# Kernel optimization log

Hardware: AMD Instinct MI355X
Metric: run time of the kernel (lower is better)

The kernel has to match this reference:

```python
import jax, jax.numpy as jnp
import numpy as np

B, S, D, H = 4, 2048, 1024, 16  # batch, seq, num_hiddens, heads
HD = D // H  # head dim = 64
MASK_VALUE = -1e6


def setup_inputs() -> dict:
    key = jax.random.key(0)
    ks = jax.random.split(key, 8)
    scale = 1.0 / np.sqrt(D)
    return {
        "queries": jax.random.normal(ks[0], (B, S, D), jnp.float32),
        "keys": jax.random.normal(ks[1], (B, S, D), jnp.float32),
        "values": jax.random.normal(ks[2], (B, S, D), jnp.float32),
        "valid_lens": jax.random.randint(ks[3], (B,), 1, S + 1, jnp.int32),
        # torch Linear weights: shape (out_features, in_features), y = x @ W.T
        "Wq": jax.random.uniform(ks[4], (D, D), jnp.float32, -scale, scale),
        "Wk": jax.random.uniform(ks[5], (D, D), jnp.float32, -scale, scale),
        "Wv": jax.random.uniform(ks[6], (D, D), jnp.float32, -scale, scale),
        "Wo": jax.random.uniform(ks[7], (D, D), jnp.float32, -scale, scale),
    }


def _split_heads(x):
    # (B, S, D) -> (B, H, S, HD)
    return x.reshape(B, S, H, HD).transpose(0, 2, 1, 3)


def reference(queries, keys, values, valid_lens, Wq, Wk, Wv, Wo):
    q = _split_heads(queries @ Wq.T)
    k = _split_heads(keys @ Wk.T)
    v = _split_heads(values @ Wv.T)
    scores = jnp.einsum("bhqd,bhkd->bhqk", q, k) / jnp.sqrt(jnp.float32(HD))
    # per-batch valid_len masks keys beyond valid_len (same for all heads/queries)
    key_pos = jnp.arange(S)
    mask = key_pos[None, None, None, :] < valid_lens[:, None, None, None]
    scores = jnp.where(mask, scores, MASK_VALUE)
    attn = jax.nn.softmax(scores, axis=-1)
    out = jnp.einsum("bhqk,bhkd->bhqd", attn, v)  # (B, H, S, HD)
    out = out.transpose(0, 2, 1, 3).reshape(B, S, D)
    return out @ Wo.T
```

## Files before the change

### kernel.cpp

```cpp
#include <hip/hip_runtime.h>

#define Bn 4
#define Sn 2048
#define Dn 1024
#define Hn 16
#define HDn 64

typedef unsigned short u16;
typedef unsigned int u32;
typedef __bf16 bf16x8 __attribute__((ext_vector_type(8)));
typedef float f32x4 __attribute__((ext_vector_type(4)));

__device__ __forceinline__ u32 pack_rne(float a, float b) {
    u32 ua = __float_as_uint(a); ua += 0x7fffu + ((ua >> 16) & 1u);
    u32 ub = __float_as_uint(b); ub += 0x7fffu + ((ub >> 16) & 1u);
    return __builtin_amdgcn_perm(ub, ua, 0x07060302u);
}
__device__ __forceinline__ u32 pack_trunc(float a, float b) {
    return __builtin_amdgcn_perm(__float_as_uint(b), __float_as_uint(a), 0x07060302u);
}

__device__ __forceinline__ void async_copy16(const u16* g, u16* l) {
    __builtin_amdgcn_global_load_lds(
        (__attribute__((address_space(1))) void*)(g),
        (__attribute__((address_space(3))) void*)(l), 16, 0, 0);
}

struct CvtArgs {
    const float* in[7];
    u16* out[7];
    int n4[7];
};
__global__ __launch_bounds__(256) void cvt_multi(CvtArgs a) {
    int s = blockIdx.y;
    const float4* in4 = (const float4*)a.in[s];
    uint2* out2 = (uint2*)a.out[s];
    int n4 = a.n4[s];
    int i = blockIdx.x * blockDim.x + threadIdx.x;
    int stride = gridDim.x * blockDim.x;
    for (; i < n4; i += stride) {
        float4 v = in4[i];
        out2[i] = make_uint2(pack_rne(v.x, v.y), pack_rne(v.z, v.w));
    }
}

struct GemmArgs {
    const u16* A[3];
    const u16* Bw[3];
    void* C[3];
    float scale[3];
    int mode[3];
};
template <int NZ>
__global__ __launch_bounds__(256, 3) void gemm_bf16(GemmArgs g) {
    __shared__ alignas(16) u16 As[128 * 64];
    __shared__ alignas(16) u16 Bs[128 * 64];
    u32 id = blockIdx.x;
    int xcd = id & 7;
    u32 s = id >> 3;
    int col0 = (int)(s & 7) * 128;
    u32 t2 = s >> 3;
    int z = (int)(t2 % NZ);
    int rg = (int)(t2 / NZ);
    int row0 = (rg * 8 + xcd) * 128;

    const u16* A = g.A[z];
    const u16* Bw = g.Bw[z];
    void* Cout = g.C[z];
    float scale = g.scale[z];
    int mode = g.mode[z];

    int t = threadIdx.x;
    int w = t >> 6, lane = t & 63;
    int lane15 = lane & 15, quad = lane >> 4;
    int wr = w >> 1, wc = w & 1;
    int sr = t >> 3, sg = t & 7;

    bool swapped = (mode != 3);
    const u16* PA = swapped ? Bs : As;
    const u16* PB = swapped ? As : Bs;
    int abase = swapped ? wc * 64 : wr * 64;
    int bbase = swapped ? wr * 64 : wc * 64;

    f32x4 acc[4][4];
#pragma unroll
    for (int mt = 0; mt < 4; ++mt)
#pragma unroll
        for (int nt = 0; nt < 4; ++nt)
            acc[mt][nt] = f32x4{0.f, 0.f, 0.f, 0.f};

    for (int k0 = 0; k0 < 1024; k0 += 64) {
        __syncthreads();
#pragma unroll
        for (int i = 0; i < 4; ++i) {
            int r = i * 32 + sr;
            int gc = ((sg ^ (r & 7)) << 3);
            const u16* ga = A + (size_t)(row0 + r) * 1024 + k0 + gc;
            const u16* gb = Bw + (size_t)(col0 + r) * 1024 + k0 + gc;
            async_copy16(ga, &As[i * 2048 + w * 512]);
            async_copy16(gb, &Bs[i * 2048 + w * 512]);
        }
        __syncthreads();

#pragma unroll
        for (int kc = 0; kc < 2; ++kc) {
            bf16x8 af[4], bf[4];
#pragma unroll
            for (int mt = 0; mt < 4; ++mt) {
                int r = abase + mt * 16 + lane15;
                af[mt] = *(const bf16x8*)&PA[r * 64 + (((kc * 4 + quad) ^ (r & 7)) << 3)];
            }
#pragma unroll
            for (int nt = 0; nt < 4; ++nt) {
                int r = bbase + nt * 16 + lane15;
                bf[nt] = *(const bf16x8*)&PB[r * 64 + (((kc * 4 + quad) ^ (r & 7)) << 3)];
            }
#pragma unroll
            for (int mt = 0; mt < 4; ++mt)
#pragma unroll
                for (int nt = 0; nt < 4; ++nt)
                    acc[mt][nt] = __builtin_amdgcn_mfma_f32_16x16x32_bf16(
                        af[mt], bf[nt], acc[mt][nt], 0, 0, 0);
        }
    }

#pragma unroll
    for (int mt = 0; mt < 4; ++mt)
#pragma unroll
        for (int nt = 0; nt < 4; ++nt) {
            if (mode == 1) {
                int f0 = col0 + wc * 64 + mt * 16 + quad * 4;
                int tok = row0 + wr * 64 + nt * 16 + lane15;
                int bb = tok >> 11, ss = tok & 2047;
                int hh = f0 >> 6, dd = f0 & 63;
                u32 w0 = pack_rne(acc[mt][nt][0] * scale, acc[mt][nt][1] * scale);
                u32 w1 = pack_rne(acc[mt][nt][2] * scale, acc[mt][nt][3] * scale);
                u16* p = (u16*)Cout + (((size_t)bb * Hn + hh) * Sn + ss) * HDn + dd;
                *(uint2*)p = make_uint2(w0, w1);
            } else if (mode == 2) {
                int f0 = col0 + wc * 64 + mt * 16 + quad * 4;
                int tok = row0 + wr * 64 + nt * 16 + lane15;
                float4 o = make_float4(acc[mt][nt][0] * scale, acc[mt][nt][1] * scale,
                                       acc[mt][nt][2] * scale, acc[mt][nt][3] * scale);
                *(float4*)((float*)Cout + (size_t)tok * 1024 + f0) = o;
            } else {
                int n = col0 + wc * 64 + nt * 16 + lane15;
                int m0 = row0 + wr * 64 + mt * 16 + quad * 4;
                int bb = m0 >> 11, ss = m0 & 2047;
                int hh = n >> 6, dd = n & 63;
                u32 w0 = pack_rne(acc[mt][nt][0] * scale, acc[mt][nt][1] * scale);
                u32 w1 = pack_rne(acc[mt][nt][2] * scale, acc[mt][nt][3] * scale);
                u16* p = (u16*)Cout + (((size_t)bb * Hn + hh) * HDn + dd) * Sn + ss;
                *(uint2*)p = make_uint2(w0, w1);
            }
        }
}

__global__ __launch_bounds__(256, 4) void attn_kernel(const u16* __restrict__ Qh,
                                                      const u16* __restrict__ Kh,
                                                      const u16* __restrict__ Vtg,
                                                      const int* __restrict__ valid_lens,
                                                      u16* __restrict__ O) {
    __shared__ alignas(16) u16 Ks[64 * 72];
    __shared__ alignas(16) u16 Vt[64 * 72];

    int t = threadIdx.x;
    int w = t >> 6, lane = t & 63;
    int lane15 = lane & 15, quad = lane >> 4;

    u32 raw = blockIdx.x;
    int qt = raw >> 6;
    int h = (raw >> 2) & 15;
    int b = (raw & 3) ^ ((raw >> 8) & 3);
    int bh = b * Hn + h;
    int q0 = qt * 128;
    int vl = valid_lens[b];
    int ntiles = (vl + 63) >> 6;

    const u16* Qb = Qh + (size_t)bh * (Sn * HDn);
    const u16* Kb = Kh + (size_t)bh * (Sn * HDn);
    const u16* Vb = Vtg + (size_t)bh * (HDn * Sn);

    int sr = t >> 3;
    int sc8 = (t & 7) * 8;
    int va = t & 7;
    int vcb = ((va & 4) << 3) | ((va & 1) << 4) | ((va & 2) << 1);

    bf16x8 qf[2][2];
#pragma unroll
    for (int nt = 0; nt < 2; ++nt)
#pragma unroll
        for (int kc = 0; kc < 2; ++kc)
            qf[nt][kc] = *(const bf16x8*)(Qb + (size_t)(q0 + w * 32 + nt * 16 + lane15) * HDn +
                                          kc * 32 + quad * 8);

    f32x4 oacc[4][2], lacc[2];
#pragma unroll
    for (int mt = 0; mt < 4; ++mt)
#pragma unroll
        for (int nt = 0; nt < 2; ++nt)
            oacc[mt][nt] = f32x4{0.f, 0.f, 0.f, 0.f};
    lacc[0] = f32x4{0.f, 0.f, 0.f, 0.f};
    lacc[1] = f32x4{0.f, 0.f, 0.f, 0.f};

    union { u32 u[4]; bf16x8 v; } ones;
    ones.u[0] = ones.u[1] = ones.u[2] = ones.u[3] = 0x3F803F80u;

    uint4 kpre[2], vpre[2];
#pragma unroll
    for (int p = 0; p < 2; ++p) {
        kpre[p] = *(const uint4*)(Kb + (size_t)(p * 32 + sr) * HDn + sc8);
        vpre[p] = *(const uint4*)(Vb + (size_t)(p * 32 + sr) * Sn + sc8);
    }

    for (int kt = 0; kt < ntiles; ++kt) {
        int kbase = kt * 64;
        __syncthreads();
#pragma unroll
        for (int p = 0; p < 2; ++p) {
            *(uint4*)&Ks[(p * 32 + sr) * 72 + sc8] = kpre[p];
            int drow = (p * 32 + sr) * 72;
            *(uint2*)&Vt[drow + vcb] = make_uint2(vpre[p].x, vpre[p].y);
            *(uint2*)&Vt[drow + vcb + 8] = make_uint2(vpre[p].z, vpre[p].w);
        }
        __syncthreads();

        int nkb = (kt + 1 < ntiles) ? kbase + 64 : kbase;
#pragma unroll
        for (int p = 0; p < 2; ++p) {
            kpre[p] = *(const uint4*)(Kb + (size_t)(nkb + p * 32 + sr) * HDn + sc8);
            vpre[p] = *(const uint4*)(Vb + (size_t)(p * 32 + sr) * Sn + nkb + sc8);
        }

        f32x4 sc[4][2];
#pragma unroll
        for (int mt = 0; mt < 4; ++mt) {
            bf16x8 kf0 = *(const bf16x8*)&Ks[(mt * 16 + lane15) * 72 + quad * 8];
            bf16x8 kf1 = *(const bf16x8*)&Ks[(mt * 16 + lane15) * 72 + 32 + quad * 8];
#pragma unroll
            for (int nt = 0; nt < 2; ++nt) {
                f32x4 s = f32x4{0.f, 0.f, 0.f, 0.f};
                s = __builtin_amdgcn_mfma_f32_16x16x32_bf16(kf0, qf[nt][0], s, 0, 0, 0);
                s = __builtin_amdgcn_mfma_f32_16x16x32_bf16(kf1, qf[nt][1], s, 0, 0, 0);
                sc[mt][nt] = s;
            }
        }

        if (kbase + 64 > vl) {
#pragma unroll
            for (int mt = 0; mt < 4; ++mt)
#pragma unroll
                for (int reg = 0; reg < 4; ++reg) {
                    int key = kbase + mt * 16 + quad * 4 + reg;
                    if (key >= vl) {
                        sc[mt][0][reg] = -1e30f;
                        sc[mt][1][reg] = -1e30f;
                    }
                }
        }

#pragma unroll
        for (int mt = 0; mt < 4; ++mt)
#pragma unroll
            for (int nt = 0; nt < 2; ++nt)
#pragma unroll
                for (int reg = 0; reg < 4; ++reg)
                    sc[mt][nt][reg] = __builtin_amdgcn_exp2f(sc[mt][nt][reg]);

        union { u32 u[4]; bf16x8 v; } pv[2][2];
#pragma unroll
        for (int nt = 0; nt < 2; ++nt) {
            pv[nt][0].u[0] = pack_trunc(sc[0][nt][0], sc[0][nt][1]);
            pv[nt][0].u[1] = pack_trunc(sc[0][nt][2], sc[0][nt][3]);
            pv[nt][0].u[2] = pack_trunc(sc[1][nt][0], sc[1][nt][1]);
            pv[nt][0].u[3] = pack_trunc(sc[1][nt][2], sc[1][nt][3]);
            pv[nt][1].u[0] = pack_trunc(sc[2][nt][0], sc[2][nt][1]);
            pv[nt][1].u[1] = pack_trunc(sc[2][nt][2], sc[2][nt][3]);
            pv[nt][1].u[2] = pack_trunc(sc[3][nt][0], sc[3][nt][1]);
            pv[nt][1].u[3] = pack_trunc(sc[3][nt][2], sc[3][nt][3]);
            lacc[nt] = __builtin_amdgcn_mfma_f32_16x16x32_bf16(
                ones.v, pv[nt][0].v, lacc[nt], 0, 0, 0);
            lacc[nt] = __builtin_amdgcn_mfma_f32_16x16x32_bf16(
                ones.v, pv[nt][1].v, lacc[nt], 0, 0, 0);
        }

#pragma unroll
        for (int mt = 0; mt < 4; ++mt) {
            bf16x8 vf0 = *(const bf16x8*)&Vt[(mt * 16 + lane15) * 72 + quad * 8];
            bf16x8 vf1 = *(const bf16x8*)&Vt[(mt * 16 + lane15) * 72 + 32 + quad * 8];
#pragma unroll
            for (int nt = 0; nt < 2; ++nt) {
                oacc[mt][nt] = __builtin_amdgcn_mfma_f32_16x16x32_bf16(
                    vf0, pv[nt][0].v, oacc[mt][nt], 0, 0, 0);
                oacc[mt][nt] = __builtin_amdgcn_mfma_f32_16x16x32_bf16(
                    vf1, pv[nt][1].v, oacc[mt][nt], 0, 0, 0);
            }
        }
    }

    float rl[2];
    rl[0] = __builtin_amdgcn_rcpf(lacc[0][0]);
    rl[1] = __builtin_amdgcn_rcpf(lacc[1][0]);
#pragma unroll
    for (int mt = 0; mt < 4; ++mt)
#pragma unroll
        for (int nt = 0; nt < 2; ++nt) {
            int q = q0 + w * 32 + nt * 16 + lane15;
            int d = h * HDn + mt * 16 + quad * 4;
            u32 w0 = pack_rne(oacc[mt][nt][0] * rl[nt], oacc[mt][nt][1] * rl[nt]);
            u32 w1 = pack_rne(oacc[mt][nt][2] * rl[nt], oacc[mt][nt][3] * rl[nt]);
            *(uint2*)&O[((size_t)b * Sn + q) * Dn + d] = make_uint2(w0, w1);
        }
}

extern "C" void kernel_launch(void* const* d_in, const int* in_sizes, int n_in,
                              void* d_out, int out_size, void* d_ws, size_t ws_size,
                              hipStream_t stream) {
    const float* q  = (const float*)d_in[0];
    const float* k  = (const float*)d_in[1];
    const float* v  = (const float*)d_in[2];
    const int*   vl = (const int*)d_in[3];
    const float* Wq = (const float*)d_in[4];
    const float* Wk = (const float*)d_in[5];
    const float* Wv = (const float*)d_in[6];
    const float* Wo = (const float*)d_in[7];

    u16* ws = (u16*)d_ws;
    const size_t NE = (size_t)Bn * Sn * Dn;
    const size_t NW = (size_t)Dn * Dn;
    const float qscale = 0.125f * 1.44269504f;

    if (ws_size >= (6 * NE + 4 * NW) * 2) {
        u16* Qh  = ws;
        u16* Kh  = Qh + NE;
        u16* Vh  = Kh + NE;
        u16* Xq  = Vh + NE;
        u16* Xk  = Xq + NE;
        u16* Xv  = Xk + NE;
        u16* Wqb = Xv + NE;
        u16* Wkb = Wqb + NW;
        u16* Wvb = Wkb + NW;
        u16* Wob = Wvb + NW;
        u16* Ob  = Xq;

        CvtArgs ca;
        ca.in[0] = q;  ca.out[0] = Xq;  ca.n4[0] = (int)(NE / 4);
        ca.in[1] = k;  ca.out[1] = Xk;  ca.n4[1] = (int)(NE / 4);
        ca.in[2] = v;  ca.out[2] = Xv;  ca.n4[2] = (int)(NE / 4);
        ca.in[3] = Wq; ca.out[3] = Wqb; ca.n4[3] = (int)(NW / 4);
        ca.in[4] = Wk; ca.out[4] = Wkb; ca.n4[4] = (int)(NW / 4);
        ca.in[5] = Wv; ca.out[5] = Wvb; ca.n4[5] = (int)(NW / 4);
        ca.in[6] = Wo; ca.out[6] = Wob; ca.n4[6] = (int)(NW / 4);
        cvt_multi<<<dim3(512, 7), 256, 0, stream>>>(ca);

        GemmArgs gp;
        gp.A[0] = Xq; gp.Bw[0] = Wqb; gp.C[0] = Qh; gp.scale[0] = qscale; gp.mode[0] = 1;
        gp.A[1] = Xk; gp.Bw[1] = Wkb; gp.C[1] = Kh; gp.scale[1] = 1.0f;   gp.mode[1] = 1;
        gp.A[2] = Xv; gp.Bw[2] = Wvb; gp.C[2] = Vh; gp.scale[2] = 1.0f;   gp.mode[2] = 3;
        gemm_bf16<3><<<dim3(1536), 256, 0, stream>>>(gp);

        attn_kernel<<<dim3(1024), 256, 0, stream>>>(Qh, Kh, Vh, vl, Ob);

        GemmArgs go;
        for (int i = 0; i < 3; ++i) {
            go.A[i] = Ob; go.Bw[i] = Wob; go.C[i] = d_out;
            go.scale[i] = 1.0f; go.mode[i] = 2;
        }
        gemm_bf16<1><<<dim3(512), 256, 0, stream>>>(go);
    } else {
        u16* Qh  = ws;
        u16* Kh  = Qh + NE;
        u16* Vh  = Kh + NE;
        u16* Xb  = Vh + NE;
        u16* Wqb = Xb + NE;
        u16* Wkb = Wqb + NW;
        u16* Wvb = Wkb + NW;
        u16* Wob = Wvb + NW;
        u16* Ob  = Wob + NW;

        CvtArgs cw;
        cw.in[0] = Wq; cw.out[0] = Wqb; cw.n4[0] = (int)(NW / 4);
        cw.in[1] = Wk; cw.out[1] = Wkb; cw.n4[1] = (int)(NW / 4);
        cw.in[2] = Wv; cw.out[2] = Wvb; cw.n4[2] = (int)(NW / 4);
        cw.in[3] = Wo; cw.out[3] = Wob; cw.n4[3] = (int)(NW / 4);
        for (int i = 4; i < 7; ++i) { cw.in[i] = Wq; cw.out[i] = Wqb; cw.n4[i] = 0; }
        cvt_multi<<<dim3(512, 4), 256, 0, stream>>>(cw);

        const float* xs[3] = {q, k, v};
        u16* outs[3] = {Qh, Kh, Vh};
        const u16* wbs[3] = {Wqb, Wkb, Wvb};
        float scs[3] = {qscale, 1.0f, 1.0f};
        int mds[3] = {1, 1, 3};
        for (int i = 0; i < 3; ++i) {
            CvtArgs cx;
            cx.in[0] = xs[i]; cx.out[0] = Xb; cx.n4[0] = (int)(NE / 4);
            for (int j = 1; j < 7; ++j) { cx.in[j] = xs[i]; cx.out[j] = Xb; cx.n4[j] = 0; }
            cvt_multi<<<dim3(512, 1), 256, 0, stream>>>(cx);
            GemmArgs gp;
            for (int j = 0; j < 3; ++j) {
                gp.A[j] = Xb; gp.Bw[j] = wbs[i]; gp.C[j] = outs[i];
                gp.scale[j] = scs[i]; gp.mode[j] = mds[i];
            }
            gemm_bf16<1><<<dim3(512), 256, 0, stream>>>(gp);
        }

        attn_kernel<<<dim3(1024), 256, 0, stream>>>(Qh, Kh, Vh, vl, Ob);

        GemmArgs go;
        for (int j = 0; j < 3; ++j) {
            go.A[j] = Ob; go.Bw[j] = Wob; go.C[j] = d_out;
            go.scale[j] = 1.0f; go.mode[j] = 2;
        }
        gemm_bf16<1><<<dim3(512), 256, 0, stream>>>(go);
    }
}
```

Baseline: 312.1 us.

## Fuse fp32 activation conversion into QKV GEMM and shrink attention query tile

The QKV projection GEMM now reads fp32 activations directly, converts them to bf16 in registers and writes them to LDS. The next k-slice is prefetched into registers while the MFMAs run. This removes the separate conversion pass over the three large activation tensors and its extra global traffic. The attention kernel now processes 64 queries per block instead of 128, launches twice as many blocks with a higher occupancy hint, and remaps blocks to batch-head. The out-projection gets its own specialised GEMM and the fallback workspace path is dropped. The trade-offs are that the A-operand load is now synchronous rather than an async copy to LDS, and each K/V tile loaded in attention serves fewer queries.

```diff
diff --git a/kernel.cpp b/kernel.cpp
--- a/kernel.cpp
+++ b/kernel.cpp
@@ -27,9 +27,9 @@
 }
 
 struct CvtArgs {
-    const float* in[7];
-    u16* out[7];
-    int n4[7];
+    const float* in[4];
+    u16* out[4];
+    int n4[4];
 };
 __global__ __launch_bounds__(256) void cvt_multi(CvtArgs a) {
     int s = blockIdx.y;
@@ -44,15 +44,14 @@
     }
 }
 
-struct GemmArgs {
-    const u16* A[3];
+struct QkvArgs {
+    const float* A[3];
     const u16* Bw[3];
-    void* C[3];
+    u16* C[3];
     float scale[3];
     int mode[3];
 };
-template <int NZ>
-__global__ __launch_bounds__(256, 3) void gemm_bf16(GemmArgs g) {
+__global__ __launch_bounds__(256, 3) void gemm_qkv(QkvArgs g) {
     __shared__ alignas(16) u16 As[128 * 64];
     __shared__ alignas(16) u16 Bs[128 * 64];
     u32 id = blockIdx.x;
@@ -60,13 +59,13 @@
     u32 s = id >> 3;
     int col0 = (int)(s & 7) * 128;
     u32 t2 = s >> 3;
-    int z = (int)(t2 % NZ);
-    int rg = (int)(t2 / NZ);
+    int z = (int)(t2 % 3);
+    int rg = (int)(t2 / 3);
     int row0 = (rg * 8 + xcd) * 128;
 
-    const u16* A = g.A[z];
+    const float* A = g.A[z];
     const u16* Bw = g.Bw[z];
-    void* Cout = g.C[z];
+    u16* Cout = g.C[z];
     float scale = g.scale[z];
     int mode = g.mode[z];
 
@@ -89,18 +88,44 @@
         for (int nt = 0; nt < 4; ++nt)
             acc[mt][nt] = f32x4{0.f, 0.f, 0.f, 0.f};
 
+    float4 apre[4][2];
+#pragma unroll
+    for (int i = 0; i < 4; ++i) {
+        int r = i * 32 + sr;
+        int gc = ((sg ^ (r & 7)) << 3);
+        const float* ga = A + (size_t)(row0 + r) * 1024 + gc;
+        apre[i][0] = *(const float4*)ga;
+        apre[i][1] = *(const float4*)(ga + 4);
+    }
+
     for (int k0 = 0; k0 < 1024; k0 += 64) {
         __syncthreads();
 #pragma unroll
         for (int i = 0; i < 4; ++i) {
             int r = i * 32 + sr;
             int gc = ((sg ^ (r & 7)) << 3);
-            const u16* ga = A + (size_t)(row0 + r) * 1024 + k0 + gc;
-            const u16* gb = Bw + (size_t)(col0 + r) * 1024 + k0 + gc;
-            async_copy16(ga, &As[i * 2048 + w * 512]);
-            async_copy16(gb, &Bs[i * 2048 + w * 512]);
-        }
-        __syncthreads();
+            async_copy16(Bw + (size_t)(col0 + r) * 1024 + k0 + gc,
+                         &Bs[i * 2048 + w * 512]);
+        }
+#pragma unroll
+        for (int i = 0; i < 4; ++i) {
+            uint4 pk = make_uint4(pack_rne(apre[i][0].x, apre[i][0].y),
+                                  pack_rne(apre[i][0].z, apre[i][0].w),
+                                  pack_rne(apre[i][1].x, apre[i][1].y),
+                                  pack_rne(apre[i][1].z, apre[i][1].w));
+            *(uint4*)&As[i * 2048 + t * 8] = pk;
+        }
+        __syncthreads();
+
+        int kn = (k0 + 64 < 1024) ? k0 + 64 : k0;
+#pragma unroll
+        for (int i = 0; i < 4; ++i) {
+            int r = i * 32 + sr;
+            int gc = ((sg ^ (r & 7)) << 3);
+            const float* ga = A + (size_t)(row0 + r) * 1024 + kn + gc;
+            apre[i][0] = *(const float4*)ga;
+            apre[i][1] = *(const float4*)(ga + 4);
+        }
 
 #pragma unroll
         for (int kc = 0; kc < 2; ++kc) {
@@ -135,14 +160,8 @@
                 int hh = f0 >> 6, dd = f0 & 63;
                 u32 w0 = pack_rne(acc[mt][nt][0] * scale, acc[mt][nt][1] * scale);
                 u32 w1 = pack_rne(acc[mt][nt][2] * scale, acc[mt][nt][3] * scale);
-                u16* p = (u16*)Cout + (((size_t)bb * Hn + hh) * Sn + ss) * HDn + dd;
+                u16* p = Cout + (((size_t)bb * Hn + hh) * Sn + ss) * HDn + dd;
                 *(uint2*)p = make_uint2(w0, w1);
-            } else if (mode == 2) {
-                int f0 = col0 + wc * 64 + mt * 16 + quad * 4;
-                int tok = row0 + wr * 64 + nt * 16 + lane15;
-                float4 o = make_float4(acc[mt][nt][0] * scale, acc[mt][nt][1] * scale,
-                                       acc[mt][nt][2] * scale, acc[mt][nt][3] * scale);
-                *(float4*)((float*)Cout + (size_t)tok * 1024 + f0) = o;
             } else {
                 int n = col0 + wc * 64 + nt * 16 + lane15;
                 int m0 = row0 + wr * 64 + mt * 16 + quad * 4;
@@ -150,13 +169,83 @@
                 int hh = n >> 6, dd = n & 63;
                 u32 w0 = pack_rne(acc[mt][nt][0] * scale, acc[mt][nt][1] * scale);
                 u32 w1 = pack_rne(acc[mt][nt][2] * scale, acc[mt][nt][3] * scale);
-                u16* p = (u16*)Cout + (((size_t)bb * Hn + hh) * HDn + dd) * Sn + ss;
+                u16* p = Cout + (((size_t)bb * Hn + hh) * HDn + dd) * Sn + ss;
                 *(uint2*)p = make_uint2(w0, w1);
             }
         }
 }
 
-__global__ __launch_bounds__(256, 4) void attn_kernel(const u16* __restrict__ Qh,
+__global__ __launch_bounds__(256, 3) void gemm_out(const u16* __restrict__ A,
+                                                   const u16* __restrict__ Bw,
+                                                   float* __restrict__ Cout) {
+    __shared__ alignas(16) u16 As[128 * 64];
+    __shared__ alignas(16) u16 Bs[128 * 64];
+    u32 id = blockIdx.x;
+    int xcd = id & 7;
+    u32 s = id >> 3;
+    int col0 = (int)(s & 7) * 128;
+    int rg = (int)(s >> 3);
+    int row0 = (rg * 8 + xcd) * 128;
+
+    int t = threadIdx.x;
+    int w = t >> 6, lane = t & 63;
+    int lane15 = lane & 15, quad = lane >> 4;
+    int wr = w >> 1, wc = w & 1;
+    int sr = t >> 3, sg = t & 7;
+
+    f32x4 acc[4][4];
+#pragma unroll
+    for (int mt = 0; mt < 4; ++mt)
+#pragma unroll
+        for (int nt = 0; nt < 4; ++nt)
+            acc[mt][nt] = f32x4{0.f, 0.f, 0.f, 0.f};
+
+    for (int k0 = 0; k0 < 1024; k0 += 64) {
+        __syncthreads();
+#pragma unroll
+        for (int i = 0; i < 4; ++i) {
+            int r = i * 32 + sr;
+            int gc = ((sg ^ (r & 7)) << 3);
+            async_copy16(A + (size_t)(row0 + r) * 1024 + k0 + gc, &As[i * 2048 + w * 512]);
+            async_copy16(Bw + (size_t)(col0 + r) * 1024 + k0 + gc, &Bs[i * 2048 + w * 512]);
+        }
+        __syncthreads();
+
+#pragma unroll
+        for (int kc = 0; kc < 2; ++kc) {
+            bf16x8 af[4], bf[4];
+#pragma unroll
+            for (int mt = 0; mt < 4; ++mt) {
+                int r = wc * 64 + mt * 16 + lane15;
+                af[mt] = *(const bf16x8*)&Bs[r * 64 + (((kc * 4 + quad) ^ (r & 7)) << 3)];
+            }
+#pragma unroll
+            for (int nt = 0; nt < 4; ++nt) {
+                int r = wr * 64 + nt * 16 + lane15;
+                bf[nt] = *(const bf16x8*)&As[r * 64 + (((kc * 4 + quad) ^ (r & 7)) << 3)];
+            }
+#pragma unroll
+            for (int mt = 0; mt < 4; ++mt)
+#pragma unroll
+                for (int nt = 0; nt < 4; ++nt)
+                    acc[mt][nt] = __builtin_amdgcn_mfma_f32_16x16x32_bf16(
+                        af[mt], bf[nt], acc[mt][nt], 0, 0, 0);
+        }
+    }
+
+#pragma unroll
+    for (int mt = 0; mt < 4; ++mt)
+#pragma unroll
+        for (int nt = 0; nt < 4; ++nt) {
+            int f0 = col0 + wc * 64 + mt * 16 + quad * 4;
+            int tok = row0 + wr * 64 + nt * 16 + lane15;
+            float4 o = make_float4(acc[mt][nt][0], acc[mt][nt][1],
+                                   acc[mt][nt][2], acc[mt][nt][3]);
+            *(float4*)(Cout + (size_t)tok * 1024 + f0) = o;
+        }
+}
+
+__global__ __launch_bounds__(256, 6) void attn_kernel(const u16* __restrict__ Qh,
                                                       const u16* __restrict__ Kh,
                                                       const u16* __restrict__ Vtg,
                                                       const int* __restrict__ valid_lens,
@@ -169,11 +258,10 @@
     int lane15 = lane & 15, quad = lane >> 4;
 
     u32 raw = blockIdx.x;
-    int qt = raw >> 6;
-    int h = (raw >> 2) & 15;
-    int b = (raw & 3) ^ ((raw >> 8) & 3);
-    int bh = b * Hn + h;
-    int q0 = qt * 128;
+    int bh = (int)(raw & 7) + 8 * (int)((raw >> 3) & 7);
+    int qt = (int)(raw >> 6);
+    int b = bh >> 4, h = bh & 15;
+    int q0 = qt * 64;
     int vl = valid_lens[b];
     int ntiles = (vl + 63) >> 6;
 
@@ -186,22 +274,16 @@
     int va = t & 7;
     int vcb = ((va & 4) << 3) | ((va & 1) << 4) | ((va & 2) << 1);
 
-    bf16x8 qf[2][2];
-#pragma unroll
-    for (int nt = 0; nt < 2; ++nt)
-#pragma unroll
-        for (int kc = 0; kc < 2; ++kc)
-            qf[nt][kc] = *(const bf16x8*)(Qb + (size_t)(q0 + w * 32 + nt * 16 + lane15) * HDn +
-                                          kc * 32 + quad * 8);
-
-    f32x4 oacc[4][2], lacc[2];
-#pragma unroll
-    for (int mt = 0; mt < 4; ++mt)
-#pragma unroll
-        for (int nt = 0; nt < 2; ++nt)
-            oacc[mt][nt] = f32x4{0.f, 0.f, 0.f, 0.f};
-    lacc[0] = f32x4{0.f, 0.f, 0.f, 0.f};
-    lacc[1] = f32x4{0.f, 0.f, 0.f, 0.f};
+    bf16x8 qf[2];
+#pragma unroll
+    for (int kc = 0; kc < 2; ++kc)
+        qf[kc] = *(const bf16x8*)(Qb + (size_t)(q0 + w * 16 + lane15) * HDn +
+                                  kc * 32 + quad * 8);
+
+    f32x4 oacc[4], lacc;
+#pragma unroll
+    for (int mt = 0; mt < 4; ++mt) oacc[mt] = f32x4{0.f, 0.f, 0.f, 0.f};
+    lacc = f32x4{0.f, 0.f, 0.f, 0.f};
 
     union { u32 u[4]; bf16x8 v; } ones;
     ones.u[0] = ones.u[1] = ones.u[2] = ones.u[3] = 0x3F803F80u;
@@ -232,18 +314,15 @@
             vpre[p] = *(const uint4*)(Vb + (size_t)(p * 32 + sr) * Sn + nkb + sc8);
         }
 
-        f32x4 sc[4][2];
+        f32x4 sc[4];
 #pragma unroll
         for (int mt = 0; mt < 4; ++mt) {
             bf16x8 kf0 = *(const bf16x8*)&Ks[(mt * 16 + lane15) * 72 + quad * 8];
             bf16x8 kf1 = *(const bf16x8*)&Ks[(mt * 16 + lane15) * 72 + 32 + quad * 8];
-#pragma unroll
-            for (int nt = 0; nt < 2; ++nt) {
-                f32x4 s = f32x4{0.f, 0.f, 0.f, 0.f};
-                s = __builtin_amdgcn_mfma_f32_16x16x32_bf16(kf0, qf[nt][0], s, 0, 0, 0);
-                s = __builtin_amdgcn_mfma_f32_16x16x32_bf16(kf1, qf[nt][1], s, 0, 0, 0);
-                sc[mt][nt] = s;
-            }
+            f32x4 sv = f32x4{0.f, 0.f, 0.f, 0.f};
+            sv = __builtin_amdgcn_mfma_f32_16x16x32_bf16(kf0, qf[0], sv, 0, 0, 0);
+            sv = __builtin_amdgcn_mfma_f32_16x16x32_bf16(kf1, qf[1], sv, 0, 0, 0);
+            sc[mt] = sv;
         }
 
         if (kbase + 64 > vl) {
@@ -252,65 +331,47 @@
 #pragma unroll
                 for (int reg = 0; reg < 4; ++reg) {
                     int key = kbase + mt * 16 + quad * 4 + reg;
-                    if (key >= vl) {
-                        sc[mt][0][reg] = -1e30f;
-                        sc[mt][1][reg] = -1e30f;
-                    }
+                    if (key >= vl) sc[mt][reg] = -1e30f;
                 }
         }
 
 #pragma unroll
         for (int mt = 0; mt < 4; ++mt)
 #pragma unroll
-            for (int nt = 0; nt < 2; ++nt)
-#pragma unroll
-                for (int reg = 0; reg < 4; ++reg)
-                    sc[mt][nt][reg] = __builtin_amdgcn_exp2f(sc[mt][nt][reg]);
-
-        union { u32 u[4]; bf16x8 v; } pv[2][2];
-#pragma unroll
-        for (int nt = 0; nt < 2; ++nt) {
-            pv[nt][0].u[0] = pack_trunc(sc[0][nt][0], sc[0][nt][1]);
-            pv[nt][0].u[1] = pack_trunc(sc[0][nt][2], sc[0][nt][3]);
-            pv[nt][0].u[2] = pack_trunc(sc[1][nt][0], sc[1][nt][1]);
-            pv[nt][0].u[3] = pack_trunc(sc[1][nt][2], sc[1][nt][3]);
-            pv[nt][1].u[0] = pack_trunc(sc[2][nt][0], sc[2][nt][1]);
-            pv[nt][1].u[1] = pack_trunc(sc[2][nt][2], sc[2][nt][3]);
-            pv[nt][1].u[2] = pack_trunc(sc[3][nt][0], sc[3][nt][1]);
-            pv[nt][1].u[3] = pack_trunc(sc[3][nt][2], sc[3][nt][3]);
-            lacc[nt] = __builtin_amdgcn_mfma_f32_16x16x32_bf16(
-                ones.v, pv[nt][0].v, lacc[nt], 0, 0, 0);
-            lacc[nt] = __builtin_amdgcn_mfma_f32_16x16x32_bf16(
-                ones.v, pv[nt][1].v, lacc[nt], 0, 0, 0);
-        }
+            for (int reg = 0; reg < 4; ++reg)
+                sc[mt][reg] = __builtin_amdgcn_exp2f(sc[mt][reg]);
+
+        union { u32 u[4]; bf16x8 v; } pv0, pv1;
+        pv0.u[0] = pack_trunc(sc[0][0], sc[0][1]);
+        pv0.u[1] = pack_trunc(sc[0][2], sc[0][3]);
+        pv0.u[2] = pack_trunc(sc[1][0], sc[1][1]);
+        pv0.u[3] = pack_trunc(sc[1][2], sc[1][3]);
+        pv1.u[0] = pack_trunc(sc[2][0], sc[2][1]);
+        pv1.u[1] = pack_trunc(sc[2][2], sc[2][3]);
+        pv1.u[2] = pack_trunc(sc[3][0], sc[3][1]);
+        pv1.u[3] = pack_trunc(sc[3][2], sc[3][3]);
+
+        lacc = __builtin_amdgcn_mfma_f32_16x16x32_bf16(ones.v, pv0.v, lacc, 0, 0, 0);
+        lacc = __builtin_amdgcn_mfma_f32_16x16x32_bf16(ones.v, pv1.v, lacc, 0, 0, 0);
 
 #pragma unroll
         for (int mt = 0; mt < 4; ++mt) {
             bf16x8 vf0 = *(const bf16x8*)&Vt[(mt * 16 + lane15) * 72 + quad * 8];
             bf16x8 vf1 = *(const bf16x8*)&Vt[(mt * 16 + lane15) * 72 + 32 + quad * 8];
-#pragma unroll
-            for (int nt = 0; nt < 2; ++nt) {
-                oacc[mt][nt] = __builtin_amdgcn_mfma_f32_16x16x32_bf16(
-                    vf0, pv[nt][0].v, oacc[mt][nt], 0, 0, 0);
-                oacc[mt][nt] = __builtin_amdgcn_mfma_f32_16x16x32_bf16(
-                    vf1, pv[nt][1].v, oacc[mt][nt], 0, 0, 0);
-            }
-        }
-    }
-
-    float rl[2];
-    rl[0] = __builtin_amdgcn_rcpf(lacc[0][0]);
-    rl[1] = __builtin_amdgcn_rcpf(lacc[1][0]);
-#pragma unroll
-    for (int mt = 0; mt < 4; ++mt)
-#pragma unroll
-        for (int nt = 0; nt < 2; ++nt) {
-            int q = q0 + w * 32 + nt * 16 + lane15;
-            int d = h * HDn + mt * 16 + quad * 4;
-            u32 w0 = pack_rne(oacc[mt][nt][0] * rl[nt], oacc[mt][nt][1] * rl[nt]);
-            u32 w1 = pack_rne(oacc[mt][nt][2] * rl[nt], oacc[mt][nt][3] * rl[nt]);
-            *(uint2*)&O[((size_t)b * Sn + q) * Dn + d] = make_uint2(w0, w1);
-        }
+            oacc[mt] = __builtin_amdgcn_mfma_f32_16x16x32_bf16(vf0, pv0.v, oacc[mt], 0, 0, 0);
+            oacc[mt] = __builtin_amdgcn_mfma_f32_16x16x32_bf16(vf1, pv1.v, oacc[mt], 0, 0, 0);
+        }
+    }
+
+    float rl = __builtin_amdgcn_rcpf(lacc[0]);
+    int q = q0 + w * 16 + lane15;
+#pragma unroll
+    for (int mt = 0; mt < 4; ++mt) {
+        int d = h * HDn + mt * 16 + quad * 4;
+        u32 w0 = pack_rne(oacc[mt][0] * rl, oacc[mt][1] * rl);
+        u32 w1 = pack_rne(oacc[mt][2] * rl, oacc[mt][3] * rl);
+        *(uint2*)&O[((size_t)b * Sn + q) * Dn + d] = make_uint2(w0, w1);
+    }
 }
 
 extern "C" void kernel_launch(void* const* d_in, const int* in_sizes, int n_in,
@@ -330,87 +391,29 @@
     const size_t NW = (size_t)Dn * Dn;
     const float qscale = 0.125f * 1.44269504f;
 
-    if (ws_size >= (6 * NE + 4 * NW) * 2) {
-        u16* Qh  = ws;
-        u16* Kh  = Qh + NE;
-        u16* Vh  = Kh + NE;
-        u16* Xq  = Vh + NE;
-        u16* Xk  = Xq + NE;
-        u16* Xv  = Xk + NE;
-        u16* Wqb = Xv + NE;
-        u16* Wkb = Wqb + NW;
-        u16* Wvb = Wkb + NW;
-        u16* Wob = Wvb + NW;
-        u16* Ob  = Xq;
-
-        CvtArgs ca;
-        ca.in[0] = q;  ca.out[0] = Xq;  ca.n4[0] = (int)(NE / 4);
-        ca.in[1] = k;  ca.out[1] = Xk;  ca.n4[1] = (int)(NE / 4);
-        ca.in[2] = v;  ca.out[2] = Xv;  ca.n4[2] = (int)(NE / 4);
-        ca.in[3] = Wq; ca.out[3] = Wqb; ca.n4[3] = (int)(NW / 4);
-        ca.in[4] = Wk; ca.out[4] = Wkb; ca.n4[4] = (int)(NW / 4);
-        ca.in[5] = Wv; ca.out[5] = Wvb; ca.n4[5] = (int)(NW / 4);
-        ca.in[6] = Wo; ca.out[6] = Wob; ca.n4[6] = (int)(NW / 4);
-        cvt_multi<<<dim3(512, 7), 256, 0, stream>>>(ca);
-
-        GemmArgs gp;
-        gp.A[0] = Xq; gp.Bw[0] = Wqb; gp.C[0] = Qh; gp.scale[0] = qscale; gp.mode[0] = 1;
-        gp.A[1] = Xk; gp.Bw[1] = Wkb; gp.C[1] = Kh; gp.scale[1] = 1.0f;   gp.mode[1] = 1;
-        gp.A[2] = Xv; gp.Bw[2] = Wvb; gp.C[2] = Vh; gp.scale[2] = 1.0f;   gp.mode[2] = 3;
-        gemm_bf16<3><<<dim3(1536), 256, 0, stream>>>(gp);
-
-        attn_kernel<<<dim3(1024), 256, 0, stream>>>(Qh, Kh, Vh, vl, Ob);
-
-        GemmArgs go;
-        for (int i = 0; i < 3; ++i) {
-            go.A[i] = Ob; go.Bw[i] = Wob; go.C[i] = d_out;
-            go.scale[i] = 1.0f; go.mode[i] = 2;
-        }
-        gemm_bf16<1><<<dim3(512), 256, 0, stream>>>(go);
-    } else {
-        u16* Qh  = ws;
-        u16* Kh  = Qh + NE;
-        u16* Vh  = Kh + NE;
-        u16* Xb  = Vh + NE;
-        u16* Wqb = Xb + NE;
-        u16* Wkb = Wqb + NW;
-        u16* Wvb = Wkb + NW;
-        u16* Wob = Wvb + NW;
-        u16* Ob  = Wob + NW;
-
-        CvtArgs cw;
-        cw.in[0] = Wq; cw.out[0] = Wqb; cw.n4[0] = (int)(NW / 4);
-        cw.in[1] = Wk; cw.out[1] = Wkb; cw.n4[1] = (int)(NW / 4);
-        cw.in[2] = Wv; cw.out[2] = Wvb; cw.n4[2] = (int)(NW / 4);
-        cw.in[3] = Wo; cw.out[3] = Wob; cw.n4[3] = (int)(NW / 4);
-        for (int i = 4; i < 7; ++i) { cw.in[i] = Wq; cw.out[i] = Wqb; cw.n4[i] = 0; }
-        cvt_multi<<<dim3(512, 4), 256, 0, stream>>>(cw);
-
-        const float* xs[3] = {q, k, v};
-        u16* outs[3] = {Qh, Kh, Vh};
-        const u16* wbs[3] = {Wqb, Wkb, Wvb};
-        float scs[3] = {qscale, 1.0f, 1.0f};
-        int mds[3] = {1, 1, 3};
-        for (int i = 0; i < 3; ++i) {
-            CvtArgs cx;
-            cx.in[0] = xs[i]; cx.out[0] = Xb; cx.n4[0] = (int)(NE / 4);
-            for (int j = 1; j < 7; ++j) { cx.in[j] = xs[i]; cx.out[j] = Xb; cx.n4[j] = 0; }
-            cvt_multi<<<dim3(512, 1), 256, 0, stream>>>(cx);
-            GemmArgs gp;
-            for (int j = 0; j < 3; ++j) {
-                gp.A[j] = Xb; gp.Bw[j] = wbs[i]; gp.C[j] = outs[i];
-                gp.scale[j] = scs[i]; gp.mode[j] = mds[i];
-            }
-            gemm_bf16<1><<<dim3(512), 256, 0, stream>>>(gp);
-        }
-
-        attn_kernel<<<dim3(1024), 256, 0, stream>>>(Qh, Kh, Vh, vl, Ob);
-
-        GemmArgs go;
-        for (int j = 0; j < 3; ++j) {
-            go.A[j] = Ob; go.Bw[j] = Wob; go.C[j] = d_out;
-            go.scale[j] = 1.0f; go.mode[j] = 2;
-        }
-        gemm_bf16<1><<<dim3(512), 256, 0, stream>>>(go);
-    }
-}
+    u16* Qh  = ws;
+    u16* Kh  = Qh + NE;
+    u16* Vh  = Kh + NE;
+    u16* Ob  = Vh + NE;
+    u16* Wqb = Ob + NE;
+    u16* Wkb = Wqb + NW;
+    u16* Wvb = Wkb + NW;
+    u16* Wob = Wvb + NW;
+
+    CvtArgs cw;
+    cw.in[0] = Wq; cw.out[0] = Wqb; cw.n4[0] = (int)(NW / 4);
+    cw.in[1] = Wk; cw.out[1] = Wkb; cw.n4[1] = (int)(NW / 4);
+    cw.in[2] = Wv; cw.out[2] = Wvb; cw.n4[2] = (int)(NW / 4);
+    cw.in[3] = Wo; cw.out[3] = Wob; cw.n4[3] = (int)(NW / 4);
+    cvt_multi<<<dim3(256, 4), 256, 0, stream>>>(cw);
+
+    QkvArgs gp;
+    gp.A[0] = q; gp.Bw[0] = Wqb; gp.C[0] = Qh; gp.scale[0] = qscale; gp.mode[0] = 1;
+    gp.A[1] = k; gp.Bw[1] = Wkb; gp.C[1] = Kh; gp.scale[1] = 1.0f;   gp.mode[1] = 1;
+    gp.A[2] = v; gp.Bw[2] = Wvb; gp.C[2] = Vh; gp.scale[2] = 1.0f;   gp.mode[2] = 3;
+    gemm_qkv<<<dim3(1536), 256, 0, stream>>>(gp);
+
+    attn_kernel<<<dim3(2048), 256, 0, stream>>>(Qh, Kh, Vh, vl, Ob);
+
+    gemm_out<<<dim3(512), 256, 0, stream>>>(Ob, Wob, (float*)d_out);
+}
```

Measured after the change: 471.8 us. 1.51x slower.
